# Optimization experiments

Measured on AMD Instinct MI355X. Metric: run time of the kernel, lower is better.

Reference implementation:

```python
import jax, jax.numpy as jnp
import numpy as np

V, D, H, L, F, S, B = 32000, 1024, 16, 6, 4096, 1024, 2
DK = D // H
SCALE = float(np.sqrt(DK))
NEG = -1e9


def _make_pe(max_len, d_model):
    pos = np.arange(max_len, dtype=np.float32)[:, None]
    div = np.exp(np.arange(0, d_model, 2, dtype=np.float32) * (-np.log(10000.0) / d_model))
    pe = np.zeros((max_len, d_model), dtype=np.float32)
    pe[:, 0::2] = np.sin(pos * div)
    pe[:, 1::2] = np.cos(pos * div)
    return jnp.asarray(pe)


def _ln(x, g, b, eps=1e-5):
    m = x.mean(-1, keepdims=True)
    v = ((x - m) ** 2).mean(-1, keepdims=True)
    return (x - m) / jnp.sqrt(v + eps) * g + b


def setup_inputs() -> dict:
    key = jax.random.key(0)
    ks = jax.random.split(key, 10)
    std = 0.02
    tokens = jax.random.randint(ks[0], (B, S), 0, V)
    emb = (jax.random.normal(ks[1], (V, D)) * std).at[0].set(0.0)  # padding_idx=0 row zeroed
    pe = _make_pe(4096, D)
    Wq = jax.random.normal(ks[2], (L, D, D)) * std
    Wk = jax.random.normal(ks[3], (L, D, D)) * std
    Wv = jax.random.normal(ks[4], (L, D, D)) * std
    Wo = jax.random.normal(ks[5], (L, D, D)) * std
    bo = jnp.zeros((L, D))
    g1 = jnp.ones((L, D)); be1 = jnp.zeros((L, D))
    g2 = jnp.ones((L, D)); be2 = jnp.zeros((L, D))
    W1 = jax.random.normal(ks[6], (L, D, F)) * std
    b1 = jnp.zeros((L, F))
    W2 = jax.random.normal(ks[7], (L, F, D)) * std
    b2 = jnp.zeros((L, D))
    gf = jnp.ones((D,)); bf = jnp.zeros((D,))
    Wout = jax.random.normal(ks[8], (D, V)) * std
    bout = jnp.zeros((V,))
    return dict(tokens=tokens, emb=emb, pe=pe, Wq=Wq, Wk=Wk, Wv=Wv, Wo=Wo, bo=bo,
                g1=g1, be1=be1, g2=g2, be2=be2, W1=W1, b1=b1, W2=W2, b2=b2,
                gf=gf, bf=bf, Wout=Wout, bout=bout)


def reference(tokens, emb, pe, Wq, Wk, Wv, Wo, bo, g1, be1, g2, be2,
              W1, b1, W2, b2, gf, bf, Wout, bout):
    Bx, Sx = tokens.shape
    x = emb[tokens] * jnp.sqrt(jnp.float32(D)) + pe[:Sx]  # (B,S,D)
    pad = tokens == 0  # (B,S) padding mask
    causal = jnp.triu(jnp.ones((Sx, Sx), dtype=bool), 1)
    mask = causal[None, None] | pad[:, None, None, :]  # (B,1,S,S), True = masked
    for l in range(L):
        h = _ln(x, g1[l], be1[l])
        q = (h @ Wq[l]).reshape(Bx, Sx, H, DK)
        k = (h @ Wk[l]).reshape(Bx, Sx, H, DK)
        v = (h @ Wv[l]).reshape(Bx, Sx, H, DK)
        scores = jnp.einsum('bqhd,bkhd->bhqk', q, k) / SCALE
        scores = jnp.where(mask, NEG, scores)  # masked_fill(mask, -1e9)
        a = jax.nn.softmax(scores, axis=-1)
        ctx = jnp.einsum('bhqk,bkhd->bqhd', a, v).reshape(Bx, Sx, D)
        x = x + ctx @ Wo[l] + bo[l]
        h = _ln(x, g2[l], be2[l])
        x = x + jax.nn.gelu(h @ W1[l] + b1[l], approximate=False) @ W2[l] + b2[l]
    x = _ln(x, gf, bf)
    return x @ Wout + bout  # (B,S,V)
```

## Files before the change

kernel.cpp:

```cpp
#include <hip/hip_runtime.h>
#include <hip/hip_bf16.h>
#include <stdint.h>

typedef __hip_bfloat16 bf16;
typedef __attribute__((ext_vector_type(8))) short bf16x8;
typedef __attribute__((ext_vector_type(4))) float f32x4;

#define DEV static __device__ __forceinline__

DEV float b2f(bf16 v) { return __bfloat162float(v); }
DEV bf16  f2b(float v) { return __float2bfloat16(v); }

DEV void gload16(const void* g, void* l) {
  __builtin_amdgcn_global_load_lds(
      (__attribute__((address_space(1))) void*)(void*)g,
      (__attribute__((address_space(3))) void*)l, 16, 0, 0);
}

DEV f32x4 mfma16(bf16x8 a, bf16x8 b, f32x4 c) {
  return __builtin_amdgcn_mfma_f32_16x16x32_bf16(a, b, c, 0, 0, 0);
}

__global__ __launch_bounds__(256) void embed_kernel(
    const int* __restrict__ tok, const float* __restrict__ emb,
    const float* __restrict__ pe, float* __restrict__ x)
{
  const int r = blockIdx.x, t = threadIdx.x;
  const int s = r & 1023;
  const int tk = tok[r];
  const int d = t * 4;
  const float* ep = emb + (size_t)tk * 1024 + d;
  const float* pp = pe + (size_t)s * 1024 + d;
  float* xp = x + (size_t)r * 1024 + d;
  #pragma unroll
  for (int j = 0; j < 4; ++j)
    xp[j] = ep[j] * 32.0f + pp[j];
}

__global__ __launch_bounds__(256) void ln_kernel(
    const float* __restrict__ x, const float* __restrict__ g,
    const float* __restrict__ be, bf16* __restrict__ h)
{
  const int r = blockIdx.x, t = threadIdx.x;
  const float4 v = ((const float4*)(x + (size_t)r * 1024))[t];
  float s  = v.x + v.y + v.z + v.w;
  float sq = v.x * v.x + v.y * v.y + v.z * v.z + v.w * v.w;
  #pragma unroll
  for (int d = 1; d < 64; d <<= 1) {
    s  += __shfl_xor(s, d);
    sq += __shfl_xor(sq, d);
  }
  __shared__ float red[8];
  const int w = t >> 6, l = t & 63;
  if (l == 0) { red[w] = s; red[4 + w] = sq; }
  __syncthreads();
  s  = red[0] + red[1] + red[2] + red[3];
  sq = red[4] + red[5] + red[6] + red[7];
  const float mean = s * (1.0f / 1024.0f);
  const float var  = sq * (1.0f / 1024.0f) - mean * mean;
  const float inv  = 1.0f / sqrtf(var + 1e-5f);
  bf16* hp = h + (size_t)r * 1024 + t * 4;
  const float* gp = g + t * 4;
  const float* bp = be + t * 4;
  const float vv[4] = {v.x, v.y, v.z, v.w};
  #pragma unroll
  for (int j = 0; j < 4; ++j)
    hp[j] = f2b((vv[j] - mean) * inv * gp[j] + bp[j]);
}

__global__ __launch_bounds__(256) void ln_res_kernel(
    float* __restrict__ x, const float* __restrict__ P, int np,
    const float* __restrict__ bias, const float* __restrict__ g,
    const float* __restrict__ be, bf16* __restrict__ h)
{
  const int r = blockIdx.x, t = threadIdx.x;
  float4 v = ((const float4*)(x + (size_t)r * 1024))[t];
  for (int i = 0; i < np; ++i) {
    const float4 pv = ((const float4*)(P + ((size_t)i * 2048 + r) * 1024))[t];
    v.x += pv.x; v.y += pv.y; v.z += pv.z; v.w += pv.w;
  }
  const float4 bv = ((const float4*)bias)[t];
  v.x += bv.x; v.y += bv.y; v.z += bv.z; v.w += bv.w;

  float s  = v.x + v.y + v.z + v.w;
  float sq = v.x * v.x + v.y * v.y + v.z * v.z + v.w * v.w;
  #pragma unroll
  for (int d = 1; d < 64; d <<= 1) {
    s  += __shfl_xor(s, d);
    sq += __shfl_xor(sq, d);
  }
  __shared__ float red[8];
  const int w = t >> 6, l = t & 63;
  if (l == 0) { red[w] = s; red[4 + w] = sq; }
  __syncthreads();
  s  = red[0] + red[1] + red[2] + red[3];
  sq = red[4] + red[5] + red[6] + red[7];
  const float mean = s * (1.0f / 1024.0f);
  const float var  = sq * (1.0f / 1024.0f) - mean * mean;
  const float inv  = 1.0f / sqrtf(var + 1e-5f);

  ((float4*)(x + (size_t)r * 1024))[t] = v;
  bf16* hp = h + (size_t)r * 1024 + t * 4;
  const float* gp = g + t * 4;
  const float* bp = be + t * 4;
  const float vv[4] = {v.x, v.y, v.z, v.w};
  #pragma unroll
  for (int j = 0; j < 4; ++j)
    hp[j] = f2b((vv[j] - mean) * inv * gp[j] + bp[j]);
}

DEV void transpose_tile(const float* __restrict__ in, bf16* __restrict__ out,
                        int ldin, int ldout, int r0, int c0, int t)
{
  __shared__ bf16 tile[64][64];
  #pragma unroll
  for (int i = 0; i < 4; ++i) {
    const int r = i * 16 + (t >> 4), c = (t & 15) * 4;
    const float4 v = *(const float4*)&in[(size_t)(r0 + r) * ldin + c0 + c];
    tile[r][c + 0] = f2b(v.x);
    tile[r][c + 1] = f2b(v.y);
    tile[r][c + 2] = f2b(v.z);
    tile[r][c + 3] = f2b(v.w);
  }
  __syncthreads();
  #pragma unroll
  for (int i = 0; i < 2; ++i) {
    const int oc = i * 32 + (t >> 3);
    const int rr = (t & 7) * 8;
    unsigned short tmp[8] __attribute__((aligned(16)));
    #pragma unroll
    for (int j = 0; j < 8; ++j)
      tmp[j] = ((const unsigned short*)tile)[(rr + j) * 64 + oc];
    *(uint4*)&out[(size_t)(c0 + oc) * ldout + r0 + rr] = *(const uint4*)tmp;
  }
}

__global__ __launch_bounds__(256) void transpose_cast_kernel(
    const float* __restrict__ in, bf16* __restrict__ out, int ldin, int ldout)
{
  transpose_tile(in, out, ldin, ldout, blockIdx.y * 64, blockIdx.x * 64, threadIdx.x);
}

DEV void prep_dispatch(int wid,
    const float* Wq, const float* Wk, const float* Wv, const float* Wo,
    const float* W1, const float* W2,
    bf16* WqkvT, bf16* WoT, bf16* W1T, bf16* W2T, int t)
{
  const float* src; bf16* dst; int ldin, ldout, tx, ty;
  if (wid < 768) {
    const int m = wid >> 8, tt = wid & 255;
    src = (m == 0) ? Wq : (m == 1) ? Wk : Wv;
    dst = WqkvT + (size_t)m * 1024 * 1024;
    ldin = 1024; ldout = 1024; tx = tt & 15; ty = tt >> 4;
  } else if (wid < 1024) {
    const int tt = wid - 768;
    src = Wo; dst = WoT; ldin = 1024; ldout = 1024; tx = tt & 15; ty = tt >> 4;
  } else if (wid < 2048) {
    const int tt = wid - 1024;
    src = W1; dst = W1T; ldin = 4096; ldout = 1024; tx = tt & 63; ty = tt >> 6;
  } else {
    const int tt = wid - 2048;
    src = W2; dst = W2T; ldin = 1024; ldout = 4096; tx = tt & 15; ty = tt >> 4;
  }
  transpose_tile(src, dst, ldin, ldout, ty * 64, tx * 64, t);
}

__global__ __launch_bounds__(256) void prep_layer_kernel(
    const float* __restrict__ Wq, const float* __restrict__ Wk,
    const float* __restrict__ Wv, const float* __restrict__ Wo,
    const float* __restrict__ W1, const float* __restrict__ W2,
    bf16* __restrict__ WqkvT, bf16* __restrict__ WoT,
    bf16* __restrict__ W1T, bf16* __restrict__ W2T)
{
  prep_dispatch(blockIdx.x, Wq, Wk, Wv, Wo, W1, W2,
                WqkvT, WoT, W1T, W2T, threadIdx.x);
}

__global__ __launch_bounds__(256) void prep_all_kernel(
    const float* __restrict__ Wq, const float* __restrict__ Wk,
    const float* __restrict__ Wv, const float* __restrict__ Wo,
    const float* __restrict__ W1, const float* __restrict__ W2,
    bf16* __restrict__ WqkvT, bf16* __restrict__ WoT,
    bf16* __restrict__ W1T, bf16* __restrict__ W2T)
{
  const int layer = blockIdx.x / 3072;
  const int wid = blockIdx.x - layer * 3072;
  const size_t DD = (size_t)1024 * 1024, DF = (size_t)1024 * 4096;
  prep_dispatch(wid,
      Wq + layer * DD, Wk + layer * DD, Wv + layer * DD, Wo + layer * DD,
      W1 + layer * DF, W2 + layer * DF,
      WqkvT + layer * 3 * DD, WoT + layer * DD,
      W1T + layer * DF, W2T + layer * DF, threadIdx.x);
}

__global__ __launch_bounds__(256) void transpose_v_kernel(
    const bf16* __restrict__ qkv, bf16* __restrict__ vT)
{
  __shared__ bf16 tile[64][64];
  const int t = threadIdx.x;
  const int s0 = blockIdx.x * 64;
  const int bh = blockIdx.y;
  const int b = bh >> 4, h = bh & 15;
  const bf16* in = qkv + (size_t)(b * 1024) * 3072 + 2048 + h * 64;
  #pragma unroll
  for (int i = 0; i < 2; ++i) {
    const int r = i * 32 + (t >> 3), c = (t & 7) * 8;
    *(uint4*)&tile[r][c] = *(const uint4*)&in[(size_t)(s0 + r) * 3072 + c];
  }
  __syncthreads();
  bf16* out = vT + (size_t)(bh * 64) * 1024;
  #pragma unroll
  for (int i = 0; i < 2; ++i) {
    const int oc = i * 32 + (t >> 3);
    const int rr = (t & 7) * 8;
    unsigned short tmp[8] __attribute__((aligned(16)));
    #pragma unroll
    for (int j = 0; j < 8; ++j)
      tmp[j] = ((const unsigned short*)tile)[(rr + j) * 64 + oc];
    *(uint4*)&out[(size_t)oc * 1024 + s0 + rr] = *(const uint4*)tmp;
  }
}

template<int EPI, int BM, int SWZ>
__global__ __launch_bounds__(256) void gemm_pl(
    const bf16* __restrict__ A, int lda,
    const bf16* __restrict__ BT, int ldb,
    void* __restrict__ Cp, int ldc,
    const float* __restrict__ bias,
    int ksl)
{
  constexpr int ABUF = BM * 32;
  constexpr int MR = BM / 32;
  __shared__ bf16 As[3 * ABUF];
  __shared__ bf16 Bs[3 * 4096];
  const int t = threadIdx.x;

  int bm, bn;
  if constexpr (SWZ) {
    const int nbm = gridDim.x;
    const int nwg = nbm * gridDim.y;
    int wid = blockIdx.x + nbm * blockIdx.y;
    wid = (wid & 7) * (nwg >> 3) + (wid >> 3);
    bm = wid % nbm; bn = wid / nbm;
  } else {
    bm = blockIdx.x; bn = blockIdx.y;
  }

  const int w = t >> 6, l = t & 63;
  const int wr = (w >> 1) * (BM / 2), wc = (w & 1) * 64;
  const int l15 = l & 15, l4 = l >> 4;
  const int kbeg = blockIdx.z * ksl;
  const int ntiles = ksl >> 5;

  const int colblk = (((t & 3) ^ ((t >> 3) & 3))) * 8;
  const bf16* gA = A  + (size_t)(bm * BM  + (t >> 2)) * lda + colblk + kbeg;
  const bf16* gB = BT + (size_t)(bn * 128 + (t >> 2)) * ldb + colblk + kbeg;
  bf16* lA = As + w * 512;
  bf16* lB = Bs + w * 512;

  auto stage = [&](int tile, int buf) {
    const int k0 = tile * 32;
    gload16(gA + k0, lA + buf * ABUF);
    if constexpr (BM == 128)
      gload16(gA + (size_t)64 * lda + k0, lA + buf * ABUF + 2048);
    gload16(gB + k0, lB + buf * 4096);
    gload16(gB + (size_t)64 * ldb + k0, lB + buf * 4096 + 2048);
  };

  f32x4 acc[MR][4];
  #pragma unroll
  for (int m = 0; m < MR; ++m)
    #pragma unroll
    for (int n = 0; n < 4; ++n)
      acc[m][n] = (f32x4){0.f, 0.f, 0.f, 0.f};

  stage(0, 0);
  stage(1, 1);

  const int rdcol = ((l4 ^ ((l15 >> 1) & 3))) * 8;

  int buf = 0;
  for (int kt = 0; kt < ntiles; ++kt) {
    if (kt + 2 < ntiles) {
      int pb = buf + 2; if (pb >= 3) pb -= 3;
      stage(kt + 2, pb);
      __builtin_amdgcn_sched_barrier(0);
      if constexpr (BM == 128) asm volatile("s_waitcnt vmcnt(8)" ::: "memory");
      else                     asm volatile("s_waitcnt vmcnt(6)" ::: "memory");
    } else if (kt + 1 < ntiles) {
      if constexpr (BM == 128) asm volatile("s_waitcnt vmcnt(4)" ::: "memory");
      else                     asm volatile("s_waitcnt vmcnt(3)" ::: "memory");
    } else {
      asm volatile("s_waitcnt vmcnt(0)" ::: "memory");
    }
    __builtin_amdgcn_s_barrier();
    __builtin_amdgcn_sched_barrier(0);

    const bf16* Ab = As + buf * ABUF;
    const bf16* Bb = Bs + buf * 4096;
    bf16x8 af[MR], bfr[4];
    #pragma unroll
    for (int m = 0; m < MR; ++m)
      af[m] = *(const bf16x8*)&Ab[(wr + m * 16 + l15) * 32 + rdcol];
    #pragma unroll
    for (int n = 0; n < 4; ++n)
      bfr[n] = *(const bf16x8*)&Bb[(wc + n * 16 + l15) * 32 + rdcol];
    #pragma unroll
    for (int m = 0; m < MR; ++m)
      #pragma unroll
      for (int n = 0; n < 4; ++n)
        acc[m][n] = mfma16(af[m], bfr[n], acc[m][n]);

    __builtin_amdgcn_sched_barrier(0);
    __builtin_amdgcn_s_barrier();
    if (++buf >= 3) buf = 0;
  }

  const int crow = bm * BM + wr, ccol = bn * 128 + wc;
  #pragma unroll
  for (int n = 0; n < 4; ++n) {
    const int col = ccol + n * 16 + l15;
    float bv = 0.f;
    if (EPI == 1 || EPI == 2) bv = bias[col];
    #pragma unroll
    for (int m = 0; m < MR; ++m) {
      const int row = crow + m * 16 + l4 * 4;
      #pragma unroll
      for (int r = 0; r < 4; ++r) {
        const float v = acc[m][n][r];
        if (EPI == 0) {
          ((bf16*)Cp)[(size_t)(row + r) * ldc + col] = f2b(v);
        } else if (EPI == 1) {
          ((float*)Cp)[(size_t)(row + r) * ldc + col] = v + bv;
        } else if (EPI == 2) {
          const float u = v + bv;
          const float gel = 0.5f * u * (1.0f + erff(u * 0.70710678118654752f));
          ((bf16*)Cp)[(size_t)(row + r) * ldc + col] = f2b(gel);
        } else {
          const int M = gridDim.x * BM;
          ((float*)Cp)[((size_t)blockIdx.z * M + row + r) * ldc + col] = v;
        }
      }
    }
  }
}

__global__ __launch_bounds__(256) void attn_kernel(
    const bf16* __restrict__ qkv, const bf16* __restrict__ vT,
    const int* __restrict__ tokens, bf16* __restrict__ ctx)
{
  __shared__ bf16 Ks[128 * 64];
  __shared__ bf16 VTs[64 * 128];
  __shared__ bf16 Ps[128 * 128];

  const int qt = blockIdx.x;
  const int bh = blockIdx.y;
  const int b = bh >> 4, h = bh & 15;
  const int t = threadIdx.x, w = t >> 6, l = t & 63;
  const int l15 = l & 15, l4 = l >> 4;
  const int q0 = qt * 128;

  bf16x8 aq[2][2];
  #pragma unroll
  for (int m = 0; m < 2; ++m)
    #pragma unroll
    for (int ks = 0; ks < 2; ++ks)
      aq[m][ks] = *(const bf16x8*)(qkv +
          (size_t)(b * 1024 + q0 + w * 32 + m * 16 + l15) * 3072 +
          h * 64 + ks * 32 + l4 * 8);

  f32x4 o[2][4];
  float m_run[2][4], l_run[2][4];
  #pragma unroll
  for (int m = 0; m < 2; ++m)
    #pragma unroll
    for (int r = 0; r < 4; ++r) { m_run[m][r] = -1e30f; l_run[m][r] = 0.f; }
  #pragma unroll
  for (int m = 0; m < 2; ++m)
    #pragma unroll
    for (int nn = 0; nn < 4; ++nn)
      o[m][nn] = (f32x4){0.f, 0.f, 0.f, 0.f};

  const bf16* kb = qkv + (size_t)(b * 1024) * 3072 + 1024 + h * 64;
  const bf16* vb = vT + (size_t)(bh * 64) * 1024;
  const int* tb = tokens + b * 1024;

  const int kSrcCol = ((t & 7) ^ ((t >> 3) & 7)) * 8;
  const int vSrcCol = ((t & 15) ^ (t >> 4)) * 8;

  for (int jt = 0; jt <= qt; ++jt) {
    const int j0 = jt * 128;
    __syncthreads();
    #pragma unroll
    for (int i = 0; i < 4; ++i)
      gload16(kb + (size_t)(j0 + i * 32 + (t >> 3)) * 3072 + kSrcCol,
              Ks + i * 2048 + w * 512);
    #pragma unroll
    for (int i = 0; i < 4; ++i)
      gload16(vb + (size_t)(i * 16 + (t >> 4)) * 1024 + j0 + vSrcCol,
              VTs + i * 2048 + w * 512);
    __syncthreads();

    f32x4 s[2][8];
    #pragma unroll
    for (int m = 0; m < 2; ++m)
      #pragma unroll
      for (int n = 0; n < 8; ++n)
        s[m][n] = (f32x4){0.f, 0.f, 0.f, 0.f};
    #pragma unroll
    for (int ks = 0; ks < 2; ++ks) {
      #pragma unroll
      for (int n = 0; n < 8; ++n) {
        const bf16x8 bk = *(const bf16x8*)
            &Ks[(n * 16 + l15) * 64 + ((ks * 32 + l4 * 8) ^ ((l15 & 7) * 8))];
        #pragma unroll
        for (int m = 0; m < 2; ++m)
          s[m][n] = mfma16(aq[m][ks], bk, s[m][n]);
      }
    }

    float padv[8];
    #pragma unroll
    for (int n = 0; n < 8; ++n)
      padv[n] = (tb[j0 + n * 16 + l15] == 0) ? 1.f : 0.f;

    #pragma unroll
    for (int m = 0; m < 2; ++m) {
      #pragma unroll
      for (int r = 0; r < 4; ++r) {
        const int rloc = l4 * 4 + r;
        const int qrow = q0 + w * 32 + m * 16 + rloc;
        float vals[8];
        float mx = -1e30f;
        #pragma unroll
        for (int n = 0; n < 8; ++n) {
          const int jg = j0 + n * 16 + l15;
          float v = s[m][n][r] * 0.125f;
          if (jg > qrow || padv[n] != 0.f) v = -1e9f;
          vals[n] = v;
          mx = fmaxf(mx, v);
        }
        #pragma unroll
        for (int d = 1; d < 16; d <<= 1) mx = fmaxf(mx, __shfl_xor(mx, d));
        const float newm = fmaxf(m_run[m][r], mx);
        const float sc = __expf(m_run[m][r] - newm);
        m_run[m][r] = newm;
        float rs = 0.f;
        #pragma unroll
        for (int n = 0; n < 8; ++n) {
          const float pv = __expf(vals[n] - newm);
          vals[n] = pv;
          rs += pv;
        }
        #pragma unroll
        for (int d = 1; d < 16; d <<= 1) rs += __shfl_xor(rs, d);
        l_run[m][r] = l_run[m][r] * sc + rs;
        #pragma unroll
        for (int nn = 0; nn < 4; ++nn) o[m][nn][r] = o[m][nn][r] * sc;
        #pragma unroll
        for (int n = 0; n < 8; ++n)
          Ps[(w * 32 + m * 16 + rloc) * 128 +
             ((n * 16 + l15) ^ (rloc * 8))] = f2b(vals[n]);
      }
    }
    __syncthreads();

    #pragma unroll
    for (int ks = 0; ks < 4; ++ks) {
      bf16x8 ap[2];
      #pragma unroll
      for (int m = 0; m < 2; ++m)
        ap[m] = *(const bf16x8*)
            &Ps[(w * 32 + m * 16 + l15) * 128 + ((ks * 32 + l4 * 8) ^ (l15 * 8))];
      #pragma unroll
      for (int nn = 0; nn < 4; ++nn) {
        const bf16x8 bv = *(const bf16x8*)
            &VTs[(nn * 16 + l15) * 128 + ((ks * 32 + l4 * 8) ^ (l15 * 8))];
        #pragma unroll
        for (int m = 0; m < 2; ++m)
          o[m][nn] = mfma16(ap[m], bv, o[m][nn]);
      }
    }
  }

  #pragma unroll
  for (int m = 0; m < 2; ++m) {
    #pragma unroll
    for (int r = 0; r < 4; ++r) {
      const float inv = 1.0f / l_run[m][r];
      const int qrow = q0 + w * 32 + m * 16 + l4 * 4 + r;
      #pragma unroll
      for (int nn = 0; nn < 4; ++nn)
        ctx[(size_t)(b * 1024 + qrow) * 1024 + h * 64 + nn * 16 + l15] =
            f2b(o[m][nn][r] * inv);
    }
  }
}

__global__ __launch_bounds__(64) void attn_fixup_kernel(
    const int* __restrict__ tokens, const bf16* __restrict__ vT,
    bf16* __restrict__ ctx)
{
  const int bh = blockIdx.x;
  const int b = bh >> 4, h = bh & 15;
  __shared__ int p0s;
  if (threadIdx.x == 0) {
    int p = 0;
    const int* tb = tokens + b * 1024;
    while (p < 1024 && tb[p] == 0) ++p;
    p0s = p;
  }
  __syncthreads();
  const int P0 = p0s;
  if (P0 == 0) return;
  const int dk = threadIdx.x;
  const bf16* vrow = vT + (size_t)(bh * 64 + dk) * 1024;
  float sum = 0.f;
  for (int sIdx = 0; sIdx < 1024; ++sIdx) sum += b2f(vrow[sIdx]);
  const bf16 mv = f2b(sum * (1.0f / 1024.0f));
  for (int q = 0; q < P0; ++q)
    ctx[(size_t)(b * 1024 + q) * 1024 + h * 64 + dk] = mv;
}

extern "C" void kernel_launch(void* const* d_in, const int* in_sizes, int n_in,
                              void* d_out, int out_size, void* d_ws, size_t ws_size,
                              hipStream_t stream)
{
  (void)in_sizes; (void)n_in; (void)out_size;
  const int*   tokens = (const int*)d_in[0];
  const float* emb  = (const float*)d_in[1];
  const float* pe   = (const float*)d_in[2];
  const float* Wq   = (const float*)d_in[3];
  const float* Wk   = (const float*)d_in[4];
  const float* Wv   = (const float*)d_in[5];
  const float* Wo   = (const float*)d_in[6];
  const float* bo   = (const float*)d_in[7];
  const float* g1   = (const float*)d_in[8];
  const float* be1  = (const float*)d_in[9];
  const float* g2   = (const float*)d_in[10];
  const float* be2  = (const float*)d_in[11];
  const float* W1   = (const float*)d_in[12];
  const float* b1   = (const float*)d_in[13];
  const float* W2   = (const float*)d_in[14];
  const float* b2   = (const float*)d_in[15];
  const float* gf   = (const float*)d_in[16];
  const float* bff  = (const float*)d_in[17];
  const float* Wout = (const float*)d_in[18];
  const float* bout = (const float*)d_in[19];
  float* out = (float*)d_out;

  char* p = (char*)d_ws;
  auto alloc = [&](size_t bytes) {
    char* q = p;
    p += (bytes + 255) & ~(size_t)255;
    return q;
  };
  float* x    = (float*)alloc((size_t)2048 * 1024 * 4);
  float* Pp   = (float*)alloc((size_t)4 * 2048 * 1024 * 4);
  bf16* h     = (bf16*)alloc((size_t)2048 * 1024 * 2);
  bf16* qkv   = (bf16*)alloc((size_t)2048 * 3072 * 2);
  bf16* vT    = (bf16*)alloc((size_t)2048 * 1024 * 2);
  bf16* ctx   = (bf16*)alloc((size_t)2048 * 1024 * 2);
  bf16* ff    = (bf16*)alloc((size_t)2048 * 4096 * 2);
  bf16* WoutT = (bf16*)alloc((size_t)32000 * 1024 * 2);

  const size_t DD = (size_t)1024 * 1024;
  const size_t DF = (size_t)1024 * 4096;

  const size_t perLayerW = (3 * DD + DD + DF + DF) * 2;
  const size_t used = (size_t)(p - (char*)d_ws);
  const bool fullprep = ws_size >= used + 6 * perLayerW + 8192;
  const int NL = fullprep ? 6 : 1;
  bf16* WqkvT = (bf16*)alloc((size_t)NL * 3 * DD * 2);
  bf16* WoT   = (bf16*)alloc((size_t)NL * DD * 2);
  bf16* W1T   = (bf16*)alloc((size_t)NL * DF * 2);
  bf16* W2T   = (bf16*)alloc((size_t)NL * DF * 2);

  if (fullprep)
    prep_all_kernel<<<6 * 3072, 256, 0, stream>>>(
        Wq, Wk, Wv, Wo, W1, W2, WqkvT, WoT, W1T, W2T);

  embed_kernel<<<2048, 256, 0, stream>>>(tokens, emb, pe, x);

  for (int l = 0; l < 6; ++l) {
    const bf16* wqkvt; const bf16* wot; const bf16* w1t; const bf16* w2t;
    if (fullprep) {
      wqkvt = WqkvT + (size_t)l * 3 * DD;
      wot   = WoT   + (size_t)l * DD;
      w1t   = W1T   + (size_t)l * DF;
      w2t   = W2T   + (size_t)l * DF;
    } else {
      prep_layer_kernel<<<3072, 256, 0, stream>>>(
          Wq + l * DD, Wk + l * DD, Wv + l * DD, Wo + l * DD,
          W1 + l * DF, W2 + l * DF, WqkvT, WoT, W1T, W2T);
      wqkvt = WqkvT; wot = WoT; w1t = W1T; w2t = W2T;
    }

    if (l == 0)
      ln_kernel<<<2048, 256, 0, stream>>>(x, g1, be1, h);
    else
      ln_res_kernel<<<2048, 256, 0, stream>>>(
          x, Pp, 4, b2 + (l - 1) * 1024, g1 + l * 1024, be1 + l * 1024, h);

    gemm_pl<0, 64, 0><<<dim3(32, 24, 1), 256, 0, stream>>>(
        h, 1024, wqkvt, 1024, qkv, 3072, (const float*)nullptr, 1024);
    transpose_v_kernel<<<dim3(16, 32), 256, 0, stream>>>(qkv, vT);
    attn_kernel<<<dim3(8, 32), 256, 0, stream>>>(qkv, vT, tokens, ctx);
    attn_fixup_kernel<<<32, 64, 0, stream>>>(tokens, vT, ctx);
    gemm_pl<3, 64, 0><<<dim3(32, 8, 2), 256, 0, stream>>>(
        ctx, 1024, wot, 1024, Pp, 1024, (const float*)nullptr, 512);
    ln_res_kernel<<<2048, 256, 0, stream>>>(
        x, Pp, 2, bo + l * 1024, g2 + l * 1024, be2 + l * 1024, h);
    gemm_pl<2, 128, 0><<<dim3(16, 32, 1), 256, 0, stream>>>(
        h, 1024, w1t, 1024, ff, 4096, b1 + l * 4096, 1024);
    gemm_pl<3, 128, 0><<<dim3(16, 8, 4), 256, 0, stream>>>(
        ff, 4096, w2t, 4096, Pp, 1024, (const float*)nullptr, 1024);
  }

  ln_res_kernel<<<2048, 256, 0, stream>>>(x, Pp, 4, b2 + 5 * 1024, gf, bff, h);
  transpose_cast_kernel<<<dim3(500, 16), 256, 0, stream>>>(Wout, WoutT, 32000, 1024);
  gemm_pl<1, 128, 1><<<dim3(16, 250, 1), 256, 0, stream>>>(
      h, 1024, WoutT, 1024, out, 32000, bout, 1024);
}
```

Baseline: 1.496 ms.

## Add 256x256-tile 512-thread GEMM for the vocab output projection

Introduces a dedicated double-buffered GEMM kernel with 256x256 output tiles, 8 waves, XOR-swizzled LDS staging and a grid remap that groups workgroups, then uses it for the final 2048x32000 logits projection. Larger tiles raise arithmetic intensity and reduce redundant global loads of A and B, and the grid remap aims to improve L2 locality. In exchange it needs large LDS (128KB) and a very large accumulator register footprint, which limits occupancy; with 1000 workgroups on the device the tile count also quantizes less finely.

```diff
diff --git a/kernel.cpp b/kernel.cpp
--- a/kernel.cpp
+++ b/kernel.cpp
@@ -341,6 +341,103 @@
           ((float*)Cp)[((size_t)blockIdx.z * M + row + r) * ldc + col] = v;
         }
       }
+    }
+  }
+}
+
+__global__ __launch_bounds__(512, 2) void gemm256(
+    const bf16* __restrict__ A, int lda,
+    const bf16* __restrict__ BT, int ldb,
+    float* __restrict__ C, int ldc,
+    const float* __restrict__ bias, int K)
+{
+  __shared__ bf16 As[2][16384];
+  __shared__ bf16 Bs[2][16384];
+  const int t = threadIdx.x;
+
+  const int nbm = gridDim.x;
+  const int nwg = nbm * gridDim.y;
+  int wid = blockIdx.x + nbm * blockIdx.y;
+  wid = (wid & 7) * (nwg >> 3) + (wid >> 3);
+  const int bm = wid % nbm, bn = wid / nbm;
+
+  const int w = t >> 6, l = t & 63;
+  const int wm = w >> 2, wn = w & 3;
+  const int l15 = l & 15, l4 = l >> 4;
+
+  const int scol = ((t & 7) ^ ((t >> 3) & 7)) * 8;
+  const bf16* gA = A  + (size_t)(bm * 256 + (t >> 3)) * lda + scol;
+  const bf16* gB = BT + (size_t)(bn * 256 + (t >> 3)) * ldb + scol;
+  const int ldst = w * 512;
+
+  auto stage = [&](int kt, int buf) {
+    const int k0 = kt * 64;
+    #pragma unroll
+    for (int i = 0; i < 4; ++i)
+      gload16(gA + (size_t)(i * 64) * lda + k0, &As[buf][i * 4096 + ldst]);
+    #pragma unroll
+    for (int i = 0; i < 4; ++i)
+      gload16(gB + (size_t)(i * 64) * ldb + k0, &Bs[buf][i * 4096 + ldst]);
+  };
+
+  f32x4 acc[8][4];
+  #pragma unroll
+  for (int m = 0; m < 8; ++m)
+    #pragma unroll
+    for (int n = 0; n < 4; ++n)
+      acc[m][n] = (f32x4){0.f, 0.f, 0.f, 0.f};
+
+  const int NT = K >> 6;
+  stage(0, 0);
+
+  const int arow = wm * 128 + l15;
+  const int brow = wn * 64 + l15;
+
+  for (int kt = 0; kt < NT; ++kt) {
+    const int buf = kt & 1;
+    if (kt + 1 < NT) {
+      stage(kt + 1, buf ^ 1);
+      __builtin_amdgcn_sched_barrier(0);
+      asm volatile("s_waitcnt vmcnt(8)" ::: "memory");
+    } else {
+      asm volatile("s_waitcnt vmcnt(0)" ::: "memory");
+    }
+    __builtin_amdgcn_s_barrier();
+    __builtin_amdgcn_sched_barrier(0);
+
+    #pragma unroll
+    for (int ks = 0; ks < 2; ++ks) {
+      const int csw = ((ks * 4 + l4) ^ (l15 & 7)) * 8;
+      bf16x8 af[8], bfr[4];
+      #pragma unroll
+      for (int m = 0; m < 8; ++m)
+        af[m] = *(const bf16x8*)&As[buf][(arow + m * 16) * 64 + csw];
+      #pragma unroll
+      for (int n = 0; n < 4; ++n)
+        bfr[n] = *(const bf16x8*)&Bs[buf][(brow + n * 16) * 64 + csw];
+      __builtin_amdgcn_s_setprio(1);
+      #pragma unroll
+      for (int m = 0; m < 8; ++m)
+        #pragma unroll
+        for (int n = 0; n < 4; ++n)
+          acc[m][n] = mfma16(af[m], bfr[n], acc[m][n]);
+      __builtin_amdgcn_s_setprio(0);
+    }
+
+    __builtin_amdgcn_sched_barrier(0);
+    __builtin_amdgcn_s_barrier();
+  }
+
+  #pragma unroll
+  for (int n = 0; n < 4; ++n) {
+    const int col = bn * 256 + wn * 64 + n * 16 + l15;
+    const float bv = bias[col];
+    #pragma unroll
+    for (int m = 0; m < 8; ++m) {
+      const int row = bm * 256 + wm * 128 + m * 16 + l4 * 4;
+      #pragma unroll
+      for (int r = 0; r < 4; ++r)
+        C[(size_t)(row + r) * ldc + col] = acc[m][n][r] + bv;
     }
   }
 }
@@ -619,6 +716,6 @@
 
   ln_res_kernel<<<2048, 256, 0, stream>>>(x, Pp, 4, b2 + 5 * 1024, gf, bff, h);
   transpose_cast_kernel<<<dim3(500, 16), 256, 0, stream>>>(Wout, WoutT, 32000, 1024);
-  gemm_pl<1, 128, 1><<<dim3(16, 250, 1), 256, 0, stream>>>(
+  gemm256<<<dim3(8, 125), 512, 0, stream>>>(
       h, 1024, WoutT, 1024, out, 32000, bout, 1024);
 }
```

New measurement: 1.493 ms. No clear change (-0.2%).
